# Optimization experiments

Hardware: AMD Instinct MI355X
Metric: run time of the kernel (lower is better)

## Reference

```python
import jax, jax.numpy as jnp
import numpy as np

EPS = 1e-5
NEG_SLOPE = 0.01  # F.leaky_relu default


def setup_inputs() -> dict:
    key = jax.random.key(0)
    k1, k2, k3, k4 = jax.random.split(key, 4)
    N, F, H = 8192, 512, 2
    inputs = jax.random.normal(k1, (N, F), dtype=jnp.float32)
    adj = jnp.zeros((N, N), dtype=jnp.float32)  # accepted but unused by the module
    # torch Linear(F, F*H, bias=False): y = x @ W with W of shape [F, F*H]
    W = jax.random.normal(k2, (F, F * H), dtype=jnp.float32) * (1.0 / np.sqrt(F))
    a_w = jax.random.normal(k3, (1,), dtype=jnp.float32)  # Linear(1,1) weight
    a_b = jax.random.normal(k4, (1,), dtype=jnp.float32)  # Linear(1,1) bias
    return {"inputs": inputs, "adj": adj, "W": W, "a_w": a_w, "a_b": a_b}


def reference(inputs, adj, W, a_w, a_b):
    # Wh, Ws = chunk(inputs @ W, 2)
    WhWs = inputs @ W                       # [N, 2F]
    Wh, Ws = jnp.split(WhWs, 2, axis=-1)    # each [N, F]
    # bias = a(ones) = a_w * 1 + a_b  (constant scalar broadcast)
    bias = (a_w + a_b)[0]
    # dense attention: tanh(Wh + Ws + bias) @ Wh^T  -> [N, N]
    scores = jnp.tanh(Wh + Ws + bias) @ Wh.T
    attn = jax.nn.softmax(scores, axis=-1)  # [N, N]
    out = attn @ Wh + inputs                # [N, F] residual
    # training-mode batch norm over node dim, no affine
    mean = jnp.mean(out, axis=0)
    var = jnp.var(out, axis=0)
    out = (out - mean) * jax.lax.rsqrt(var + EPS)
    return jnp.where(out >= 0, out, NEG_SLOPE * out)
```

## Files before the change

### kernel.cpp

```cpp
#include <hip/hip_runtime.h>

using f32x4 = float    __attribute__((ext_vector_type(4)));
using f16x8 = _Float16 __attribute__((ext_vector_type(8)));
using f16x4 = _Float16 __attribute__((ext_vector_type(4)));

__device__ __forceinline__ void gload_lds16(const void* g, void* l) {
    __builtin_amdgcn_global_load_lds(
        (__attribute__((address_space(1))) void*)(void*)g,
        (__attribute__((address_space(3))) void*)l, 16, 0, 0);
}


__global__ __launch_bounds__(256) void k_cvt_x(
    const float* __restrict__ in, _Float16* __restrict__ out) {
    int i = (blockIdx.x * 256 + threadIdx.x) * 8;
    f32x4 a = *(const f32x4*)(in + i);
    f32x4 b = *(const f32x4*)(in + i + 4);
    f16x8 o;
    #pragma unroll
    for (int j = 0; j < 4; ++j) { o[j] = (_Float16)a[j]; o[j + 4] = (_Float16)b[j]; }
    *(f16x8*)(out + i) = o;
}

__global__ __launch_bounds__(256) void k_cvtT(
    const float* __restrict__ in, _Float16* __restrict__ out, int R, int C) {
    __shared__ _Float16 tile[32][33];
    int c0 = blockIdx.x * 32, r0 = blockIdx.y * 32;
    int tx = threadIdx.x & 31, ty = threadIdx.x >> 5;
    #pragma unroll
    for (int i = ty; i < 32; i += 8)
        tile[i][tx] = (_Float16)in[(size_t)(r0 + i) * C + c0 + tx];
    __syncthreads();
    #pragma unroll
    for (int i = ty; i < 32; i += 8)
        out[(size_t)(c0 + i) * R + r0 + tx] = tile[tx][i];
}

__global__ __launch_bounds__(512, 4) void k_gemm1f(
    const _Float16* __restrict__ A, const _Float16* __restrict__ Bt,
    _Float16* __restrict__ Whh, _Float16* __restrict__ T,
    _Float16* __restrict__ WhT,
    const float* __restrict__ aw, const float* __restrict__ ab) {
    __shared__ _Float16 As[128 * 32];
    __shared__ _Float16 B0s[64 * 32];
    __shared__ _Float16 B1s[64 * 32];
    const float bias = aw[0] + ab[0];
    const int row0 = blockIdx.y * 128, col0 = blockIdx.x * 64;
    const int tid = threadIdx.x, w = tid >> 6, lane = tid & 63;
    const int wm = w >> 2, wn = w & 3;
    const int lrow = lane & 15, quad = lane >> 4;
    const int r16 = lane >> 2;
    const int kc = (((lane & 3) - ((lane >> 3) & 3)) & 3) * 8;
    const int sq = ((quad + ((lrow >> 1) & 3)) & 3) * 8;
    f32x4 acc0[4] = {}, acc1[4] = {};
    for (int k0 = 0; k0 < 512; k0 += 32) {
        gload_lds16(A + (size_t)(row0 + w * 16 + r16) * 512 + k0 + kc,
                    As + w * 512);
        if (w < 4)
            gload_lds16(Bt + (size_t)(col0 + w * 16 + r16) * 512 + k0 + kc,
                        B0s + w * 512);
        else
            gload_lds16(Bt + (size_t)(col0 + 512 + (w - 4) * 16 + r16) * 512 + k0 + kc,
                        B1s + (w - 4) * 512);
        __syncthreads();
        f16x8 af[4], b0, b1;
        #pragma unroll
        for (int i = 0; i < 4; ++i)
            af[i] = *(const f16x8*)(As + (wm * 64 + i * 16 + lrow) * 32 + sq);
        b0 = *(const f16x8*)(B0s + (wn * 16 + lrow) * 32 + sq);
        b1 = *(const f16x8*)(B1s + (wn * 16 + lrow) * 32 + sq);
        #pragma unroll
        for (int mi = 0; mi < 4; ++mi) {
            acc0[mi] = __builtin_amdgcn_mfma_f32_16x16x32_f16(af[mi], b0, acc0[mi], 0, 0, 0);
            acc1[mi] = __builtin_amdgcn_mfma_f32_16x16x32_f16(af[mi], b1, acc1[mi], 0, 0, 0);
        }
        __syncthreads();
    }
    const int col = col0 + wn * 16 + lrow;
    #pragma unroll
    for (int mi = 0; mi < 4; ++mi) {
        int rowb = row0 + wm * 64 + mi * 16 + quad * 4;
        f16x4 pw;
        #pragma unroll
        for (int r = 0; r < 4; ++r) {
            float wh = acc0[mi][r];
            float tt = tanhf(wh + acc1[mi][r] + bias);
            Whh[(size_t)(rowb + r) * 512 + col] = (_Float16)wh;
            T[(size_t)(rowb + r) * 512 + col]   = (_Float16)tt;
            pw[r] = (_Float16)wh;
        }
        *(f16x4*)(WhT + (size_t)col * 8192 + rowb) = pw;
    }
}

__global__ __launch_bounds__(512, 4) void k_gemm2(
    const _Float16* __restrict__ A,
    const _Float16* __restrict__ Bt,
    _Float16* __restrict__ Cp) {
    __shared__ _Float16 As[2 * 256 * 32];
    __shared__ _Float16 Bs[2 * 128 * 32];
    const int row0 = blockIdx.y * 256, col0 = blockIdx.x * 128;
    const int tid = threadIdx.x, w = tid >> 6, lane = tid & 63;
    const int wm = w >> 1, wn = w & 1;
    const int lrow = lane & 15, quad = lane >> 4;
    const int r16 = lane >> 2;
    const int kc = (((lane & 3) - ((lane >> 3) & 3)) & 3) * 8;
    const int sq = ((quad + ((lrow >> 1) & 3)) & 3) * 8;
    f32x4 acc[4][4] = {};
    auto stage = [&](int b, int k0) {
        _Float16* as = As + b * (256 * 32);
        _Float16* bs = Bs + b * (128 * 32);
        #pragma unroll
        for (int i = 0; i < 3; ++i) {
            int cc = w + i * 8;
            if (cc < 16)
                gload_lds16(A + (size_t)(row0 + cc * 16 + r16) * 512 + k0 + kc,
                            as + cc * 512);
            else
                gload_lds16(Bt + (size_t)(col0 + (cc - 16) * 16 + r16) * 512 + k0 + kc,
                            bs + (cc - 16) * 512);
        }
    };
    auto compute = [&](int b) {
        const _Float16* as = As + b * (256 * 32);
        const _Float16* bs = Bs + b * (128 * 32);
        f16x8 af[4], bf[4];
        #pragma unroll
        for (int i = 0; i < 4; ++i)
            af[i] = *(const f16x8*)(as + (wm * 64 + i * 16 + lrow) * 32 + sq);
        #pragma unroll
        for (int i = 0; i < 4; ++i)
            bf[i] = *(const f16x8*)(bs + (wn * 64 + i * 16 + lrow) * 32 + sq);
        #pragma unroll
        for (int mi = 0; mi < 4; ++mi)
            #pragma unroll
            for (int ni = 0; ni < 4; ++ni)
                acc[mi][ni] = __builtin_amdgcn_mfma_f32_16x16x32_f16(
                    af[mi], bf[ni], acc[mi][ni], 0, 0, 0);
    };
    stage(0, 0);
    __syncthreads();
    #pragma unroll 1
    for (int t = 1; t < 15; t += 2) {
        stage(1, t * 32);       compute(0); __syncthreads();
        stage(0, (t + 1) * 32); compute(1); __syncthreads();
    }
    stage(1, 15 * 32); compute(0); __syncthreads();
    compute(1);
    #pragma unroll
    for (int mi = 0; mi < 4; ++mi) {
        #pragma unroll
        for (int ni = 0; ni < 4; ++ni) {
            int col = col0 + wn * 64 + ni * 16 + lrow;
            #pragma unroll
            for (int r = 0; r < 4; ++r) {
                int row = row0 + wm * 64 + mi * 16 + quad * 4 + r;
                Cp[(size_t)row * 8192 + col] = (_Float16)acc[mi][ni][r];
            }
        }
    }
}

__global__ __launch_bounds__(256) void k_softmax_rows(
    _Float16* __restrict__ S, int N) {
    const int row = blockIdx.x;
    _Float16* prow = S + (size_t)row * N;
    const int t = threadIdx.x;
    float v[32];
    #pragma unroll
    for (int it = 0; it < 4; ++it) {
        f16x8 h = *(const f16x8*)(prow + (it * 256 + t) * 8);
        #pragma unroll
        for (int j = 0; j < 8; ++j) v[it * 8 + j] = (float)h[j];
    }
    float m = v[0];
    #pragma unroll
    for (int j = 1; j < 32; ++j) m = fmaxf(m, v[j]);
    #pragma unroll
    for (int off = 32; off > 0; off >>= 1) m = fmaxf(m, __shfl_xor(m, off));
    __shared__ float red[8];
    const int wid = t >> 6, lane = t & 63;
    if (lane == 0) red[wid] = m;
    __syncthreads();
    m = fmaxf(fmaxf(red[0], red[1]), fmaxf(red[2], red[3]));
    float l = 0.f;
    #pragma unroll
    for (int j = 0; j < 32; ++j) { v[j] = __expf(v[j] - m); l += v[j]; }
    #pragma unroll
    for (int off = 32; off > 0; off >>= 1) l += __shfl_xor(l, off);
    if (lane == 0) red[4 + wid] = l;
    __syncthreads();
    float rl = 1.f / (red[4] + red[5] + red[6] + red[7]);
    #pragma unroll
    for (int it = 0; it < 4; ++it) {
        f16x8 pk;
        #pragma unroll
        for (int j = 0; j < 8; ++j)
            pk[j] = (_Float16)(v[it * 8 + j] * rl);
        *(f16x8*)(prow + (it * 256 + t) * 8) = pk;
    }
}

__global__ __launch_bounds__(512, 4) void k_gemm3(
    const _Float16* __restrict__ A,
    const _Float16* __restrict__ Bt,
    float* __restrict__ Cp) {
    __shared__ _Float16 As[2 * 128 * 32];
    __shared__ _Float16 Bs[2 * 256 * 32];
    const int bid = blockIdx.x;
    const int orig = ((bid & 7) << 6) | (bid >> 3);
    const int bx = orig & 1, by = (orig >> 1) & 63, bz = orig >> 7;
    const int row0 = by * 128, col0 = bx * 256;
    const size_t zoff = (size_t)bz * 2048;
    Cp += (size_t)bz * ((size_t)8192 * 512);
    const int tid = threadIdx.x, w = tid >> 6, lane = tid & 63;
    const int wm = w >> 2, wn = w & 3;
    const int lrow = lane & 15, quad = lane >> 4;
    const int r16 = lane >> 2;
    const int kc = (((lane & 3) - ((lane >> 3) & 3)) & 3) * 8;
    const int sq = ((quad + ((lrow >> 1) & 3)) & 3) * 8;
    f32x4 acc[4][4] = {};
    auto stage = [&](int b, int k0) {
        _Float16* as = As + b * (128 * 32);
        _Float16* bs = Bs + b * (256 * 32);
        #pragma unroll
        for (int i = 0; i < 3; ++i) {
            int cc = w + i * 8;
            if (cc < 8)
                gload_lds16(A + (size_t)(row0 + cc * 16 + r16) * 8192 + zoff + k0 + kc,
                            as + cc * 512);
            else
                gload_lds16(Bt + (size_t)(col0 + (cc - 8) * 16 + r16) * 8192 + zoff + k0 + kc,
                            bs + (cc - 8) * 512);
        }
    };
    auto compute = [&](int b) {
        const _Float16* as = As + b * (128 * 32);
        const _Float16* bs = Bs + b * (256 * 32);
        f16x8 af[4], bf[4];
        #pragma unroll
        for (int i = 0; i < 4; ++i)
            af[i] = *(const f16x8*)(as + (wm * 64 + i * 16 + lrow) * 32 + sq);
        #pragma unroll
        for (int i = 0; i < 4; ++i)
            bf[i] = *(const f16x8*)(bs + (wn * 64 + i * 16 + lrow) * 32 + sq);
        #pragma unroll
        for (int mi = 0; mi < 4; ++mi)
            #pragma unroll
            for (int ni = 0; ni < 4; ++ni)
                acc[mi][ni] = __builtin_amdgcn_mfma_f32_16x16x32_f16(
                    af[mi], bf[ni], acc[mi][ni], 0, 0, 0);
    };
    stage(0, 0);
    __syncthreads();
    #pragma unroll 1
    for (int t = 1; t < 63; t += 2) {
        stage(1, t * 32);       compute(0); __syncthreads();
        stage(0, (t + 1) * 32); compute(1); __syncthreads();
    }
    stage(1, 63 * 32); compute(0); __syncthreads();
    compute(1);
    #pragma unroll
    for (int mi = 0; mi < 4; ++mi) {
        #pragma unroll
        for (int ni = 0; ni < 4; ++ni) {
            int col = col0 + wn * 64 + ni * 16 + lrow;
            #pragma unroll
            for (int r = 0; r < 4; ++r) {
                int row = row0 + wm * 64 + mi * 16 + quad * 4 + r;
                Cp[(size_t)row * 512 + col] = acc[mi][ni][r];
            }
        }
    }
}

__global__ __launch_bounds__(256) void k_reduce_stats(
    const float* __restrict__ part, const float* __restrict__ X,
    float* __restrict__ outf, float* __restrict__ cs, float* __restrict__ cq) {
    const int t = threadIdx.x;
    const int r0 = blockIdx.x * 32;
    constexpr size_t PS = (size_t)8192 * 512;
    float s0 = 0, q0 = 0, s1 = 0, q1 = 0;
    for (int r = 0; r < 32; ++r) {
        size_t base = (size_t)(r0 + r) * 512;
        float a = part[base + t] + part[PS + base + t]
                + part[2 * PS + base + t] + part[3 * PS + base + t] + X[base + t];
        float b = part[base + t + 256] + part[PS + base + t + 256]
                + part[2 * PS + base + t + 256] + part[3 * PS + base + t + 256]
                + X[base + t + 256];
        outf[base + t] = a;       outf[base + t + 256] = b;
        s0 += a; q0 += a * a; s1 += b; q1 += b * b;
    }
    atomicAdd(&cs[t], s0);       atomicAdd(&cq[t], q0);
    atomicAdd(&cs[t + 256], s1); atomicAdd(&cq[t + 256], q1);
}

__global__ __launch_bounds__(256) void k_bn_lrelu(
    const float* __restrict__ outf, const float* __restrict__ colsum,
    const float* __restrict__ colsq, float* __restrict__ out) {
    int i = (blockIdx.x * 256 + threadIdx.x) * 4;
    int c = i & 511;
    constexpr float rN = 1.f / 8192.f;
    f32x4 v = *(const f32x4*)(outf + i);
    f32x4 s = *(const f32x4*)(colsum + c);
    f32x4 q = *(const f32x4*)(colsq + c);
    f32x4 y;
    #pragma unroll
    for (int j = 0; j < 4; ++j) {
        float mean = s[j] * rN;
        float var  = q[j] * rN - mean * mean;
        float t = (v[j] - mean) * rsqrtf(var + 1e-5f);
        y[j] = (t >= 0.f) ? t : 0.01f * t;
    }
    *(f32x4*)(out + i) = y;
}

extern "C" void kernel_launch(void* const* d_in, const int* in_sizes, int n_in,
                              void* d_out, int out_size, void* d_ws, size_t ws_size,
                              hipStream_t stream) {
    const float* X  = (const float*)d_in[0];
    const float* W  = (const float*)d_in[2];
    const float* aw = (const float*)d_in[3];
    const float* ab = (const float*)d_in[4];
    float* out = (float*)d_out;

    char* ws = (char*)d_ws;
    _Float16* Xh   = (_Float16*)(ws + 0x0);
    _Float16* Wt   = (_Float16*)(ws + 0x800000);
    _Float16* T    = (_Float16*)(ws + 0x900000);
    _Float16* Whh  = (_Float16*)(ws + 0x1100000);
    _Float16* WhT  = (_Float16*)(ws + 0x1900000);
    _Float16* S    = (_Float16*)(ws + 0x2100000);
    float*    outf = (float*)   (ws + 0xA100000);
    float*    part = (float*)   (ws + 0xB100000);
    float*    cs   = (float*)   (ws + 0xF100000);
    float*    cq   = (float*)   (ws + 0xF100800);

    hipMemsetAsync(cs, 0, 4096, stream);
    k_cvt_x<<<dim3((8192 * 512) / 2048), 256, 0, stream>>>(X, Xh);
    k_cvtT<<<dim3(1024 / 32, 512 / 32), 256, 0, stream>>>(W, Wt, 512, 1024);
    k_gemm1f<<<dim3(8, 64), 512, 0, stream>>>(Xh, Wt, Whh, T, WhT, aw, ab);
    k_gemm2<<<dim3(64, 32), 512, 0, stream>>>(T, Whh, S);
    k_softmax_rows<<<dim3(8192), 256, 0, stream>>>(S, 8192);
    k_gemm3<<<dim3(512), 512, 0, stream>>>(S, WhT, part);
    k_reduce_stats<<<dim3(256), 256, 0, stream>>>(part, X, outf, cs, cq);
    k_bn_lrelu<<<dim3((8192 * 512) / 1024), 256, 0, stream>>>(outf, cs, cq, out);
}
```

Before: 525.8 us.

## Restructure GEMM main loops to prefetch two stages ahead with explicit vmcnt waits

Both double-buffered MFMA GEMM kernels now issue loads for the next two K-slices up front. Each phase waits only until its own buffer has landed (vmcnt(3)) and barriers, then reads fragments into registers. After a second barrier it refills the same buffer with the slice two steps ahead and runs the MFMAs at raised wave priority. The aim is to keep global-to-LDS loads in flight while the matrix units compute and to drop the full __syncthreads drain. In exchange it relies on hand-counted vmcnt values matching the three loads per stage, and it adds an extra barrier per phase.

```diff
diff --git a/kernel.cpp b/kernel.cpp
--- a/kernel.cpp
+++ b/kernel.cpp
@@ -121,7 +121,11 @@
                             bs + (cc - 16) * 512);
         }
     };
-    auto compute = [&](int b) {
+    auto phase = [&](int b, int knext, bool dostage, bool last) {
+        if (last) asm volatile("s_waitcnt vmcnt(0)" ::: "memory");
+        else      asm volatile("s_waitcnt vmcnt(3)" ::: "memory");
+        __builtin_amdgcn_s_barrier();
+        asm volatile("" ::: "memory");
         const _Float16* as = As + b * (256 * 32);
         const _Float16* bs = Bs + b * (128 * 32);
         f16x8 af[4], bf[4];
@@ -131,22 +135,28 @@
         #pragma unroll
         for (int i = 0; i < 4; ++i)
             bf[i] = *(const f16x8*)(bs + (wn * 64 + i * 16 + lrow) * 32 + sq);
+        asm volatile("s_waitcnt lgkmcnt(0)" ::: "memory");
+        __builtin_amdgcn_sched_barrier(0);
+        __builtin_amdgcn_s_barrier();
+        if (dostage) stage(b, knext);
+        __builtin_amdgcn_s_setprio(1);
         #pragma unroll
         for (int mi = 0; mi < 4; ++mi)
             #pragma unroll
             for (int ni = 0; ni < 4; ++ni)
                 acc[mi][ni] = __builtin_amdgcn_mfma_f32_16x16x32_f16(
                     af[mi], bf[ni], acc[mi][ni], 0, 0, 0);
+        __builtin_amdgcn_s_setprio(0);
     };
     stage(0, 0);
-    __syncthreads();
+    stage(1, 32);
     #pragma unroll 1
-    for (int t = 1; t < 15; t += 2) {
-        stage(1, t * 32);       compute(0); __syncthreads();
-        stage(0, (t + 1) * 32); compute(1); __syncthreads();
-    }
-    stage(1, 15 * 32); compute(0); __syncthreads();
-    compute(1);
+    for (int t = 0; t < 14; t += 2) {
+        phase(0, (t + 2) * 32, true, false);
+        phase(1, (t + 3) * 32, true, false);
+    }
+    phase(0, 0, false, false);
+    phase(1, 0, false, true);
     #pragma unroll
     for (int mi = 0; mi < 4; ++mi) {
         #pragma unroll
@@ -234,7 +244,11 @@
                             bs + (cc - 8) * 512);
         }
     };
-    auto compute = [&](int b) {
+    auto phase = [&](int b, int knext, bool dostage, bool last) {
+        if (last) asm volatile("s_waitcnt vmcnt(0)" ::: "memory");
+        else      asm volatile("s_waitcnt vmcnt(3)" ::: "memory");
+        __builtin_amdgcn_s_barrier();
+        asm volatile("" ::: "memory");
         const _Float16* as = As + b * (128 * 32);
         const _Float16* bs = Bs + b * (256 * 32);
         f16x8 af[4], bf[4];
@@ -244,22 +258,28 @@
         #pragma unroll
         for (int i = 0; i < 4; ++i)
             bf[i] = *(const f16x8*)(bs + (wn * 64 + i * 16 + lrow) * 32 + sq);
+        asm volatile("s_waitcnt lgkmcnt(0)" ::: "memory");
+        __builtin_amdgcn_sched_barrier(0);
+        __builtin_amdgcn_s_barrier();
+        if (dostage) stage(b, knext);
+        __builtin_amdgcn_s_setprio(1);
         #pragma unroll
         for (int mi = 0; mi < 4; ++mi)
             #pragma unroll
             for (int ni = 0; ni < 4; ++ni)
                 acc[mi][ni] = __builtin_amdgcn_mfma_f32_16x16x32_f16(
                     af[mi], bf[ni], acc[mi][ni], 0, 0, 0);
+        __builtin_amdgcn_s_setprio(0);
     };
     stage(0, 0);
-    __syncthreads();
+    stage(1, 32);
     #pragma unroll 1
-    for (int t = 1; t < 63; t += 2) {
-        stage(1, t * 32);       compute(0); __syncthreads();
-        stage(0, (t + 1) * 32); compute(1); __syncthreads();
-    }
-    stage(1, 63 * 32); compute(0); __syncthreads();
-    compute(1);
+    for (int t = 0; t < 62; t += 2) {
+        phase(0, (t + 2) * 32, true, false);
+        phase(1, (t + 3) * 32, true, false);
+    }
+    phase(0, 0, false, false);
+    phase(1, 0, false, true);
     #pragma unroll
     for (int mi = 0; mi < 4; ++mi) {
         #pragma unroll
```

Result: no change. 529.0 us (+0.6%).
